# Kernel tuning notes

Hardware: AMD Instinct MI355X
Metric: run time of the kernel (lower is better)

The kernel has to match this reference:

```python
import jax, jax.numpy as jnp
import numpy as np

EPS = 1e-5
GROUPS = 32


def _groupnorm(x, gamma, beta):
    B, C, H, W = x.shape
    xr = x.reshape(B, GROUPS, C // GROUPS, H, W)
    mu = xr.mean(axis=(2, 3, 4), keepdims=True)
    var = xr.var(axis=(2, 3, 4), keepdims=True)
    xn = ((xr - mu) * jax.lax.rsqrt(var + EPS)).reshape(B, C, H, W)
    return xn * gamma[None, :, None, None] + beta[None, :, None, None]


def _conv1x1(x, w, b):
    # x: [B,C,H,W], w: [Cout,Cin], b: [Cout]
    return jnp.einsum('bchw,oc->bohw', x, w) + b[None, :, None, None]


def setup_inputs() -> dict:
    key = jax.random.key(0)
    ks = jax.random.split(key, 11)
    B, C, H, W = 4, 64, 64, 64
    s = 0.05  # weight scale for well-conditioned softmax
    inp = {
        'x': jax.random.normal(ks[0], (B, C, H, W), jnp.float32),
        'gn_gamma': jnp.ones((C,), jnp.float32),
        'gn_beta': jnp.zeros((C,), jnp.float32),
        'wq': jax.random.normal(ks[1], (C, C), jnp.float32) * s,
        'bq': jnp.zeros((C,), jnp.float32),
        'wk': jax.random.normal(ks[2], (C, C), jnp.float32) * s,
        'bk': jnp.zeros((C,), jnp.float32),
        'wv': jax.random.normal(ks[3], (C, C), jnp.float32) * s,
        'bv': jnp.zeros((C,), jnp.float32),
        'wp': jax.random.normal(ks[4], (C, C), jnp.float32) * s,
        'bp': jnp.zeros((C,), jnp.float32),
    }
    return inp


def reference(x, gn_gamma, gn_beta, wq, bq, wk, bk, wv, bv, wp, bp):
    B, C, H, W = x.shape
    h = _groupnorm(x, gn_gamma, gn_beta)
    q = _conv1x1(h, wq, bq)
    k = _conv1x1(h, wk, bk)
    v = _conv1x1(h, wv, bv)
    # scores over all spatial positions: [B,H,W,H,W]
    scale = 1.0 / jnp.sqrt(jnp.asarray(C, x.dtype))
    w = jnp.einsum('bchw,bcHW->bhwHW', q, k) * scale
    w = jax.nn.softmax(w.reshape(B, H, W, H * W), axis=-1).reshape(B, H, W, H, W)
    h = jnp.einsum('bhwHW,bcHW->bchw', w, v)
    h = _conv1x1(h, wp, bp)
    return x + h
```

## Files before the change

kernel.cpp:

```cpp
#include <hip/hip_runtime.h>
#include <stdint.h>

#define Bn 4
#define Cn 64
#define Sn 4096
#define Gn 32

typedef float v4f __attribute__((ext_vector_type(4)));
typedef short v8s __attribute__((ext_vector_type(8)));
typedef short v4s __attribute__((ext_vector_type(4)));

#define MFMA16(a,b,c) __builtin_amdgcn_mfma_f32_16x16x32_bf16((a),(b),(c),0,0,0)

__device__ __forceinline__ float bf2f(uint16_t u){
  union { uint32_t i; float f; } x; x.i = ((uint32_t)u) << 16; return x.f;
}
__device__ __forceinline__ uint16_t f2bf(float f){
  union { float f; uint32_t i; } x; x.f = f;
  uint32_t r = x.i + 0x7fffu + ((x.i >> 16) & 1u);
  return (uint16_t)(r >> 16);
}
__device__ __forceinline__ uint16_t f2bf_trunc(float f){
  union { float f; uint32_t i; } x; x.f = f;
  return (uint16_t)(x.i >> 16);
}
__device__ __forceinline__ v8s pack8(float4 a, float4 b){
  v8s r;
  r[0]=(short)f2bf(a.x); r[1]=(short)f2bf(a.y); r[2]=(short)f2bf(a.z); r[3]=(short)f2bf(a.w);
  r[4]=(short)f2bf(b.x); r[5]=(short)f2bf(b.y); r[6]=(short)f2bf(b.z); r[7]=(short)f2bf(b.w);
  return r;
}

__global__ __launch_bounds__(256) void gn_stats(const float* __restrict__ x,
                                                float* __restrict__ stats)
{
  const int tid = threadIdx.x;
  const float* base = x + (size_t)blockIdx.x * 8192;
  float sum = 0.f, sq = 0.f;
  #pragma unroll
  for (int i = 0; i < 8; ++i) {
    float4 v = *(const float4*)(base + ((i << 8) + tid)*4);
    sum += v.x + v.y + v.z + v.w;
    sq  += v.x*v.x + v.y*v.y + v.z*v.z + v.w*v.w;
  }
  #pragma unroll
  for (int off = 1; off < 64; off <<= 1) {
    sum += __shfl_xor(sum, off);
    sq  += __shfl_xor(sq, off);
  }
  __shared__ float red[8];
  const int w = tid >> 6;
  if ((tid & 63) == 0) { red[w] = sum; red[4+w] = sq; }
  __syncthreads();
  if (tid == 0) {
    float s = red[0]+red[1]+red[2]+red[3];
    float q = red[4]+red[5]+red[6]+red[7];
    float mean = s * (1.f/8192.f);
    float var  = q * (1.f/8192.f) - mean*mean;
    stats[blockIdx.x]       = mean;
    stats[128 + blockIdx.x] = rsqrtf(fmaxf(var, 0.f) + 1e-5f);
  }
}

__global__ __launch_bounds__(256) void gn_qkv(
    const float* __restrict__ xg, const float* __restrict__ gamma,
    const float* __restrict__ beta,
    const float* __restrict__ wq, const float* __restrict__ bq,
    const float* __restrict__ wk, const float* __restrict__ bk,
    const float* __restrict__ wv, const float* __restrict__ bv,
    const float* __restrict__ stats,
    uint16_t* __restrict__ Qg, uint16_t* __restrict__ Kg, uint16_t* __restrict__ Vg)
{
  __shared__ uint16_t Hs[16*68];
  const int tid  = threadIdx.x;
  const int w    = tid >> 6;
  const int lane = tid & 63;
  const int l15  = lane & 15;
  const int quad = lane >> 4;
  const int b      = blockIdx.x >> 8;
  const int s_base = (blockIdx.x & 255) << 4;

  {
    const int c = lane;
    const int g = c >> 1;
    const float mean = stats[b*Gn + g];
    const float rstd = stats[128 + b*Gn + g];
    const float ga = gamma[c], be = beta[c];
    float4 v = *(const float4*)(xg + ((size_t)b*Cn + c)*Sn + s_base + (w << 2));
    const int r0 = w << 2;
    Hs[(r0+0)*68 + c] = f2bf((v.x - mean)*rstd*ga + be);
    Hs[(r0+1)*68 + c] = f2bf((v.y - mean)*rstd*ga + be);
    Hs[(r0+2)*68 + c] = f2bf((v.z - mean)*rstd*ga + be);
    Hs[(r0+3)*68 + c] = f2bf((v.w - mean)*rstd*ga + be);
  }
  __syncthreads();

  v8s bh0 = *(const v8s*)(Hs + l15*68 + (quad << 3));
  v8s bh1 = *(const v8s*)(Hs + l15*68 + 32 + (quad << 3));

  #pragma unroll
  for (int t = 0; t < 3; ++t) {
    const int ot   = w*3 + t;
    const int wsel = ot >> 2;
    const int o16  = (ot & 3) << 4;
    const float* Wsel = (wsel == 0) ? wq : (wsel == 1) ? wk : wv;
    const float* Bsel = (wsel == 0) ? bq : (wsel == 1) ? bk : bv;
    const float* Wr = Wsel + (o16 + l15)*64 + (quad << 3);
    v8s a0 = pack8(*(const float4*)(Wr),      *(const float4*)(Wr + 4));
    v8s a1 = pack8(*(const float4*)(Wr + 32), *(const float4*)(Wr + 36));
    v4f d = (v4f){0.f,0.f,0.f,0.f};
    d = MFMA16(a0, bh0, d);
    d = MFMA16(a1, bh1, d);
    const int s = s_base + l15;
    if (wsel <= 1) {
      v4s qv;
      #pragma unroll
      for (int r = 0; r < 4; ++r)
        qv[r] = (short)f2bf(d[r] + Bsel[o16 + (quad << 2) + r]);
      uint16_t* dst = (wsel == 0 ? Qg : Kg) + ((size_t)b*Sn + s)*64 + o16 + (quad << 2);
      *(v4s*)dst = qv;
    } else {
      #pragma unroll
      for (int r = 0; r < 4; ++r) {
        const int o = o16 + (quad << 2) + r;
        Vg[((size_t)b*Cn + o)*Sn + s] = f2bf(d[r] + Bsel[o]);
      }
    }
  }
}

__global__ __launch_bounds__(256) void attn_split(
    const uint16_t* __restrict__ Qg, const uint16_t* __restrict__ Kg,
    const uint16_t* __restrict__ Vg,
    uint16_t* __restrict__ Opart, float* __restrict__ lpart)
{
  __shared__ uint16_t KT[4096];
  __shared__ uint16_t VT[4096];
  __shared__ uint16_t Ps[4][1280];

  const int tid  = threadIdx.x;
  const int w    = tid >> 6;
  const int lane = tid & 63;
  const int l15  = lane & 15;
  const int quad = lane >> 4;
  const int qh   = w & 1;
  const int kh   = w >> 1;
  const int bx    = blockIdx.x;
  const int split = bx & 3;
  const int qt    = (bx >> 2) & 63;
  const int b     = bx >> 8;
  const int i_base = qt << 6;
  const int j0     = split << 10;

  const uint16_t* Qb = Qg + ((size_t)b*Sn + i_base)*64;
  const uint16_t* Kb = Kg + (size_t)b*Sn*64;
  const uint16_t* Vb = Vg + (size_t)b*Cn*Sn;

  v8s qf[2][2];
  #pragma unroll
  for (int t = 0; t < 2; ++t) {
    const uint16_t* qr = Qb + (size_t)((qh << 5) + (t << 4) + l15)*64;
    qf[t][0] = *(const v8s*)(qr + (quad << 3));
    qf[t][1] = *(const v8s*)(qr + 32 + (quad << 3));
  }

  const int s0 = tid, s1 = tid + 256;
  const int kr0 = ((s0 >> 7) << 4) + (s0 & 15), kc0 = ((s0 >> 6) & 1)*32 + ((s0 >> 4) & 3)*8;
  const int kr1 = ((s1 >> 7) << 4) + (s1 & 15), kc1 = ((s1 >> 6) & 1)*32 + ((s1 >> 4) & 3)*8;

  {
    *(v8s*)(KT + (s0 << 3)) = *(const v8s*)(Kb + (size_t)(j0 + kr0)*64 + kc0);
    *(v8s*)(KT + (s1 << 3)) = *(const v8s*)(Kb + (size_t)(j0 + kr1)*64 + kc1);
    *(v8s*)(VT + (s0 << 3)) = *(const v8s*)(Vb + (size_t)kr0*Sn + j0 + kc0);
    *(v8s*)(VT + (s1 << 3)) = *(const v8s*)(Vb + (size_t)kr1*Sn + j0 + kc1);
  }

  float lsum[2] = {0.f, 0.f};
  v4f o_acc[2][4];
  #pragma unroll
  for (int t = 0; t < 2; ++t)
    #pragma unroll
    for (int n = 0; n < 4; ++n) o_acc[t][n] = (v4f){0.f,0.f,0.f,0.f};

  __syncthreads();

  const float SC = 0.18033688011112042f;
  uint16_t* Pw = Ps[w];

  for (int kt = 0; kt < 16; ++kt) {
    v8s kpA, kpB, vpA, vpB;
    if (kt < 15) {
      const int jb = j0 + ((kt + 1) << 6);
      kpA = *(const v8s*)(Kb + (size_t)(jb + kr0)*64 + kc0);
      kpB = *(const v8s*)(Kb + (size_t)(jb + kr1)*64 + kc1);
      vpA = *(const v8s*)(Vb + (size_t)kr0*Sn + jb + kc0);
      vpB = *(const v8s*)(Vb + (size_t)kr1*Sn + jb + kc1);
    }

    v4f st[2][2];
    #pragma unroll
    for (int T = 0; T < 2; ++T) {
      const int rk = ((kh << 1) + T) << 1;
      v8s ka0 = *(const v8s*)(KT + ((rk + 0) << 9) + (lane << 3));
      v8s ka1 = *(const v8s*)(KT + ((rk + 1) << 9) + (lane << 3));
      #pragma unroll
      for (int t = 0; t < 2; ++t) {
        v4f acc = (v4f){0.f,0.f,0.f,0.f};
        acc = MFMA16(ka0, qf[t][0], acc);
        acc = MFMA16(ka1, qf[t][1], acc);
        st[T][t] = acc;
      }
    }

    #pragma unroll
    for (int t = 0; t < 2; ++t)
      #pragma unroll
      for (int T = 0; T < 2; ++T) {
        v4s pw;
        #pragma unroll
        for (int r = 0; r < 4; ++r) {
          const float pv = __builtin_amdgcn_exp2f(st[T][t][r]*SC);
          lsum[t] += pv;
          pw[r] = (short)f2bf_trunc(pv);
        }
        *(v4s*)(Pw + ((t << 4) + l15)*40 + (T << 4) + (quad << 2)) = pw;
      }

    __asm__ volatile("" ::: "memory");

    v8s ap[2];
    #pragma unroll
    for (int t = 0; t < 2; ++t)
      ap[t] = *(const v8s*)(Pw + ((t << 4) + l15)*40 + (quad << 3));

    #pragma unroll
    for (int n = 0; n < 4; ++n) {
      v8s vb = *(const v8s*)(VT + (((n << 1) + kh) << 9) + (lane << 3));
      #pragma unroll
      for (int t = 0; t < 2; ++t)
        o_acc[t][n] = MFMA16(ap[t], vb, o_acc[t][n]);
    }

    __syncthreads();
    if (kt < 15) {
      *(v8s*)(KT + (s0 << 3)) = kpA;
      *(v8s*)(KT + (s1 << 3)) = kpB;
      *(v8s*)(VT + (s0 << 3)) = vpA;
      *(v8s*)(VT + (s1 << 3)) = vpB;
    }
    __syncthreads();
  }

  #pragma unroll
  for (int t = 0; t < 2; ++t) {
    lsum[t] += __shfl_xor(lsum[t], 16);
    lsum[t] += __shfl_xor(lsum[t], 32);
  }

  uint16_t* Ob = Opart + ((size_t)bx*2 + kh)*4096;
  float*    lp = lpart + ((size_t)bx*2 + kh)*64;
  #pragma unroll
  for (int t = 0; t < 2; ++t) {
    #pragma unroll
    for (int n = 0; n < 4; ++n)
      #pragma unroll
      for (int r = 0; r < 4; ++r)
        Ob[((qh << 5) + (t << 4) + (quad << 2) + r)*64 + (n << 4) + l15] = f2bf(o_acc[t][n][r]);
    if (quad == 0) lp[(qh << 5) + (t << 4) + l15] = lsum[t];
  }
}

__global__ __launch_bounds__(256) void proj_res(
    const uint16_t* __restrict__ Opart, const float* __restrict__ lpart,
    const float* __restrict__ wp, const float* __restrict__ bp,
    const float* __restrict__ xg, float* __restrict__ out)
{
  __shared__ uint16_t As[16*68];
  const int tid  = threadIdx.x;
  const int w    = tid >> 6;
  const int lane = tid & 63;
  const int l15  = lane & 15;
  const int quad = lane >> 4;
  const int b      = blockIdx.x >> 8;
  const int st     = blockIdx.x & 255;
  const int qt     = st >> 2;
  const int sub    = st & 3;
  const int s_base = st << 4;

  const uint16_t* po = Opart + (size_t)((b*64 + qt)*8)*4096 + (sub << 4)*64;
  const float*    pl = lpart + ((b*64 + qt)*8)*64 + (sub << 4);

  {
    const int e = tid << 2, row = tid >> 4, col = (tid & 15) << 2;
    float lsum = 0.f;
    #pragma unroll
    for (int sp = 0; sp < 8; ++sp) lsum += pl[sp*64 + row];
    const float linv = 1.f / lsum;
    float acc[4] = {0.f,0.f,0.f,0.f};
    #pragma unroll
    for (int sp = 0; sp < 8; ++sp) {
      v4s o = *(const v4s*)(po + sp*4096 + e);
      #pragma unroll
      for (int j = 0; j < 4; ++j) acc[j] += bf2f((uint16_t)o[j]);
    }
    v4s a;
    #pragma unroll
    for (int j = 0; j < 4; ++j) a[j] = (short)f2bf(acc[j]*linv);
    *(v4s*)(As + row*68 + col) = a;
  }
  __syncthreads();

  v8s ba0 = *(const v8s*)(As + l15*68 + (quad << 3));
  v8s ba1 = *(const v8s*)(As + l15*68 + 32 + (quad << 3));

  const float* Wr = wp + ((w << 4) + l15)*64 + (quad << 3);
  v8s a0 = pack8(*(const float4*)(Wr),      *(const float4*)(Wr + 4));
  v8s a1 = pack8(*(const float4*)(Wr + 32), *(const float4*)(Wr + 36));
  v4f d = (v4f){0.f,0.f,0.f,0.f};
  d = MFMA16(a0, ba0, d);
  d = MFMA16(a1, ba1, d);
  const int s = s_base + l15;
  #pragma unroll
  for (int r = 0; r < 4; ++r) {
    const int o = (w << 4) + (quad << 2) + r;
    const size_t idx = ((size_t)b*Cn + o)*Sn + s;
    out[idx] = d[r] + bp[o] + xg[idx];
  }
}

extern "C" void kernel_launch(void* const* d_in, const int* in_sizes, int n_in,
                              void* d_out, int out_size, void* d_ws, size_t ws_size,
                              hipStream_t stream)
{
  const float* x     = (const float*)d_in[0];
  const float* gamma = (const float*)d_in[1];
  const float* beta  = (const float*)d_in[2];
  const float* wq    = (const float*)d_in[3];
  const float* bq    = (const float*)d_in[4];
  const float* wk    = (const float*)d_in[5];
  const float* bk    = (const float*)d_in[6];
  const float* wv    = (const float*)d_in[7];
  const float* bv    = (const float*)d_in[8];
  const float* wp    = (const float*)d_in[9];
  const float* bp    = (const float*)d_in[10];

  float*    stats = (float*)d_ws;
  uint16_t* Qg    = (uint16_t*)d_ws + 1024;
  uint16_t* Kg    = Qg + (size_t)Bn*Sn*Cn;
  uint16_t* Vg    = Kg + (size_t)Bn*Sn*Cn;
  uint16_t* Opart = Vg + (size_t)Bn*Sn*Cn;
  float*    lpart = (float*)(Opart + (size_t)2048*4096);
  float*    outp  = (float*)d_out;

  gn_stats  <<<128, 256, 0, stream>>>(x, stats);
  gn_qkv    <<<1024, 256, 0, stream>>>(x, gamma, beta, wq, bq, wk, bk, wv, bv,
                                       stats, Qg, Kg, Vg);
  attn_split<<<1024, 256, 0, stream>>>(Qg, Kg, Vg, Opart, lpart);
  proj_res  <<<1024, 256, 0, stream>>>(Opart, lpart, wp, bp, x, outp);
}
```

Before: 137.6 us.

## Give each wave private K/V tiles and shuffle P in registers, dropping barriers

Each wave now loads and stages its own slice of K and V into a per-wave shared-memory region, so the two block-wide barriers per key tile are removed. The softmax probabilities are packed two per 32-bit word and rearranged into MFMA operand layout with cross-lane shuffles rather than a round trip through shared memory. Launch bounds now request four blocks per CU. In exchange, each wave reloads the K and V data its neighbours also use, doubling global loads per wave, and adds eight shuffles per tile.

```diff
diff --git a/kernel.cpp b/kernel.cpp
--- a/kernel.cpp
+++ b/kernel.cpp
@@ -20,9 +20,9 @@
   uint32_t r = x.i + 0x7fffu + ((x.i >> 16) & 1u);
   return (uint16_t)(r >> 16);
 }
-__device__ __forceinline__ uint16_t f2bf_trunc(float f){
+__device__ __forceinline__ uint32_t f2bf_trunc32(float f){
   union { float f; uint32_t i; } x; x.f = f;
-  return (uint16_t)(x.i >> 16);
+  return x.i >> 16;
 }
 __device__ __forceinline__ v8s pack8(float4 a, float4 b){
   v8s r;
@@ -129,14 +129,13 @@
   }
 }
 
-__global__ __launch_bounds__(256) void attn_split(
+__global__ __launch_bounds__(256, 4) void attn_split(
     const uint16_t* __restrict__ Qg, const uint16_t* __restrict__ Kg,
     const uint16_t* __restrict__ Vg,
     uint16_t* __restrict__ Opart, float* __restrict__ lpart)
 {
-  __shared__ uint16_t KT[4096];
-  __shared__ uint16_t VT[4096];
-  __shared__ uint16_t Ps[4][1280];
+  __shared__ uint16_t KT[4][2048];
+  __shared__ uint16_t VT[4][2048];
 
   const int tid  = threadIdx.x;
   const int w    = tid >> 6;
@@ -164,15 +163,17 @@
     qf[t][1] = *(const v8s*)(qr + 32 + (quad << 3));
   }
 
-  const int s0 = tid, s1 = tid + 256;
-  const int kr0 = ((s0 >> 7) << 4) + (s0 & 15), kc0 = ((s0 >> 6) & 1)*32 + ((s0 >> 4) & 3)*8;
-  const int kr1 = ((s1 >> 7) << 4) + (s1 & 15), kc1 = ((s1 >> 6) & 1)*32 + ((s1 >> 4) & 3)*8;
-
-  {
-    *(v8s*)(KT + (s0 << 3)) = *(const v8s*)(Kb + (size_t)(j0 + kr0)*64 + kc0);
-    *(v8s*)(KT + (s1 << 3)) = *(const v8s*)(Kb + (size_t)(j0 + kr1)*64 + kc1);
-    *(v8s*)(VT + (s0 << 3)) = *(const v8s*)(Vb + (size_t)kr0*Sn + j0 + kc0);
-    *(v8s*)(VT + (s1 << 3)) = *(const v8s*)(Vb + (size_t)kr1*Sn + j0 + kc1);
+  uint16_t* KTw = KT[w];
+  uint16_t* VTw = VT[w];
+  const int hi8 = quad << 3;
+
+  #pragma unroll
+  for (int sl = 0; sl < 4; ++sl) {
+    v8s kv = *(const v8s*)(Kb + (size_t)(j0 + (kh << 5) + ((sl >> 1) << 4) + l15)*64
+                               + ((sl & 1) << 5) + hi8);
+    *(v8s*)(KTw + (sl << 9) + (lane << 3)) = kv;
+    v8s vv = *(const v8s*)(Vb + (size_t)((sl << 4) + l15)*Sn + j0 + (kh << 5) + hi8);
+    *(v8s*)(VTw + (sl << 9) + (lane << 3)) = vv;
   }
 
   float lsum[2] = {0.f, 0.f};
@@ -182,27 +183,27 @@
     #pragma unroll
     for (int n = 0; n < 4; ++n) o_acc[t][n] = (v4f){0.f,0.f,0.f,0.f};
 
-  __syncthreads();
-
   const float SC = 0.18033688011112042f;
-  uint16_t* Pw = Ps[w];
+  const int slbase = l15 + ((quad & 1) << 5);
+  const int tsel   = quad >> 1;
 
   for (int kt = 0; kt < 16; ++kt) {
-    v8s kpA, kpB, vpA, vpB;
+    v8s kp[4], vp[4];
     if (kt < 15) {
-      const int jb = j0 + ((kt + 1) << 6);
-      kpA = *(const v8s*)(Kb + (size_t)(jb + kr0)*64 + kc0);
-      kpB = *(const v8s*)(Kb + (size_t)(jb + kr1)*64 + kc1);
-      vpA = *(const v8s*)(Vb + (size_t)kr0*Sn + jb + kc0);
-      vpB = *(const v8s*)(Vb + (size_t)kr1*Sn + jb + kc1);
+      const int jn = j0 + ((kt + 1) << 6);
+      #pragma unroll
+      for (int sl = 0; sl < 4; ++sl) {
+        kp[sl] = *(const v8s*)(Kb + (size_t)(jn + (kh << 5) + ((sl >> 1) << 4) + l15)*64
+                                   + ((sl & 1) << 5) + hi8);
+        vp[sl] = *(const v8s*)(Vb + (size_t)((sl << 4) + l15)*Sn + jn + (kh << 5) + hi8);
+      }
     }
 
     v4f st[2][2];
     #pragma unroll
     for (int T = 0; T < 2; ++T) {
-      const int rk = ((kh << 1) + T) << 1;
-      v8s ka0 = *(const v8s*)(KT + ((rk + 0) << 9) + (lane << 3));
-      v8s ka1 = *(const v8s*)(KT + ((rk + 1) << 9) + (lane << 3));
+      v8s ka0 = *(const v8s*)(KTw + (((T << 1) + 0) << 9) + (lane << 3));
+      v8s ka1 = *(const v8s*)(KTw + (((T << 1) + 1) << 9) + (lane << 3));
       #pragma unroll
       for (int t = 0; t < 2; ++t) {
         v4f acc = (v4f){0.f,0.f,0.f,0.f};
@@ -212,43 +213,48 @@
       }
     }
 
-    #pragma unroll
-    for (int t = 0; t < 2; ++t)
-      #pragma unroll
-      for (int T = 0; T < 2; ++T) {
-        v4s pw;
+    uint32_t pk[2][2][2];
+    #pragma unroll
+    for (int T = 0; T < 2; ++T)
+      #pragma unroll
+      for (int t = 0; t < 2; ++t)
         #pragma unroll
-        for (int r = 0; r < 4; ++r) {
-          const float pv = __builtin_amdgcn_exp2f(st[T][t][r]*SC);
-          lsum[t] += pv;
-          pw[r] = (short)f2bf_trunc(pv);
+        for (int d = 0; d < 2; ++d) {
+          const float p0 = __builtin_amdgcn_exp2f(st[T][t][2*d]*SC);
+          const float p1 = __builtin_amdgcn_exp2f(st[T][t][2*d+1]*SC);
+          lsum[t] += p0 + p1;
+          pk[T][t][d] = f2bf_trunc32(p0) | (f2bf_trunc32(p1) << 16);
         }
-        *(v4s*)(Pw + ((t << 4) + l15)*40 + (T << 4) + (quad << 2)) = pw;
-      }
-
-    __asm__ volatile("" ::: "memory");
 
     v8s ap[2];
     #pragma unroll
-    for (int t = 0; t < 2; ++t)
-      ap[t] = *(const v8s*)(Pw + ((t << 4) + l15)*40 + (quad << 3));
+    for (int t = 0; t < 2; ++t) {
+      union { int i[4]; v8s v; } u;
+      #pragma unroll
+      for (int i2 = 0; i2 < 4; ++i2) {
+        const int sl_ = slbase + ((i2 >> 1) << 4);
+        const int v0 = __shfl((int)pk[0][t][i2 & 1], sl_, 64);
+        const int v1 = __shfl((int)pk[1][t][i2 & 1], sl_, 64);
+        u.i[i2] = tsel ? v1 : v0;
+      }
+      ap[t] = u.v;
+    }
 
     #pragma unroll
     for (int n = 0; n < 4; ++n) {
-      v8s vb = *(const v8s*)(VT + (((n << 1) + kh) << 9) + (lane << 3));
+      v8s vb = *(const v8s*)(VTw + (n << 9) + (lane << 3));
       #pragma unroll
       for (int t = 0; t < 2; ++t)
         o_acc[t][n] = MFMA16(ap[t], vb, o_acc[t][n]);
     }
 
-    __syncthreads();
     if (kt < 15) {
-      *(v8s*)(KT + (s0 << 3)) = kpA;
-      *(v8s*)(KT + (s1 << 3)) = kpB;
-      *(v8s*)(VT + (s0 << 3)) = vpA;
-      *(v8s*)(VT + (s1 << 3)) = vpB;
-    }
-    __syncthreads();
+      #pragma unroll
+      for (int sl = 0; sl < 4; ++sl) {
+        *(v8s*)(KTw + (sl << 9) + (lane << 3)) = kp[sl];
+        *(v8s*)(VTw + (sl << 9) + (lane << 3)) = vp[sl];
+      }
+    }
   }
 
   #pragma unroll
```

Result: slower. 159.6 us (+15.9%).
